# Kernel optimization log

Hardware: AMD Instinct MI355X
Metric: run time of the kernel (lower is better)

Reference implementation:

```python
import jax, jax.numpy as jnp
import numpy as np

NEG_INF = -9e15
ALPHA = 0.2  # LeakyReLU negative slope
OUT_FEATURES = 128


def setup_inputs() -> dict:
    key = jax.random.key(0)
    k1, k2, k3, k4 = jax.random.split(key, 4)
    B, N, F_in, F_out = 4, 4096, 256, OUT_FEATURES
    h = jax.random.normal(k1, (B, N, F_in), dtype=jnp.float32)
    adj = jax.random.randint(k2, (B, N, N), 0, 2, dtype=jnp.int32)
    W = jax.random.normal(k3, (F_in, F_out), dtype=jnp.float32) * 0.07
    a = jax.random.normal(k4, (2 * F_out, 1), dtype=jnp.float32) * 0.1
    return {"h": h, "adj": adj, "W": W, "a": a}


def reference(h, adj, W, a):
    # Wh: (B, N, F_out)
    Wh = jnp.einsum('bni,io->bno', h, W)
    a1 = a[:OUT_FEATURES, 0]   # (F_out,)
    a2 = a[OUT_FEATURES:, 0]   # (F_out,)
    Wh1 = Wh @ a1              # (B, N)
    Wh2 = Wh @ a2              # (B, N)
    e = Wh1[:, :, None] + Wh2[:, None, :]          # (B, N, N)
    e = jnp.where(e >= 0, e, ALPHA * e)             # LeakyReLU
    e = jnp.where(adj > 0, e, NEG_INF)              # adjacency mask
    attention = jax.nn.softmax(e, axis=-1)          # (B, N, N)
    # dropout omitted: reference runs in eval mode (training=False)
    h_prime = jnp.einsum('bnm,bmo->bno', attention, Wh)
    return jax.nn.elu(h_prime)  # concat=True
```

## Files before the change

### kernel.cpp

```cpp
#include <hip/hip_runtime.h>
#include <hip/hip_bf16.h>
#include <math.h>

typedef __attribute__((ext_vector_type(4))) float  f32x4;
typedef __attribute__((ext_vector_type(4))) int    i32x4;
typedef __attribute__((ext_vector_type(4))) unsigned u32x4;
typedef __attribute__((ext_vector_type(8))) short  s16x8;
typedef __attribute__((ext_vector_type(4))) short  s16x4;
typedef __attribute__((ext_vector_type(8))) __bf16 bf16x8;

#define LOG2E 1.4426950408889634f

__device__ __forceinline__ short f32_to_bf16_rne(float f) {
    unsigned u = __builtin_bit_cast(unsigned, f);
    u += 0x7fffu + ((u >> 16) & 1u);
    return (short)(u >> 16);
}
__device__ __forceinline__ int pack2_bf16(float f0, float f1) {
    unsigned u0 = __builtin_bit_cast(unsigned, f0) + 0x8000u;
    unsigned u1 = __builtin_bit_cast(unsigned, f1) + 0x8000u;
    return (int)((u0 >> 16) | (u1 & 0xffff0000u));
}
__device__ __forceinline__ bf16x8 as_bf16x8(s16x8 v) {
    return __builtin_bit_cast(bf16x8, v);
}
__device__ __forceinline__ bf16x8 as_bf16x8(i32x4 v) {
    return __builtin_bit_cast(bf16x8, v);
}

__global__ void k_pack(const int* __restrict__ adj, unsigned* __restrict__ bits) {
    long t = (long)blockIdx.x * 256 + threadIdx.x;
    const int* src = adj + t * 32;
    unsigned m = 0;
    #pragma unroll
    for (int c = 0; c < 8; ++c) {
        i32x4 v = *(const i32x4*)(src + c * 4);
        #pragma unroll
        for (int j = 0; j < 4; ++j)
            m |= (v[j] != 0) ? (1u << (c * 4 + j)) : 0u;
    }
    bits[t] = m;
}

__global__ void k0_wt(const float* __restrict__ W, short* __restrict__ WT) {
    int g = blockIdx.x * 256 + threadIdx.x;
    int col = g >> 6;
    int k0 = (g & 63) * 4;
    s16x4 v;
    #pragma unroll
    for (int i = 0; i < 4; ++i) v[i] = f32_to_bf16_rne(W[(k0 + i) * 128 + col]);
    *(s16x4*)(WT + col * 256 + k0) = v;
}

__global__ __launch_bounds__(256, 2) void k1_gemm(
    const float* __restrict__ h, const float* __restrict__ a,
    const short* __restrict__ WT,
    short* __restrict__ WhT, float* __restrict__ Wh1p, float* __restrict__ Tp)
{
    int l = threadIdx.x & 63;
    int w = threadIdx.x >> 6;
    int gw = blockIdx.x * 4 + w;
    int r0 = gw * 16;
    int lm = l & 15, q = l >> 4;

    f32x4 acc[8];
    #pragma unroll
    for (int ct = 0; ct < 8; ++ct) acc[ct] = (f32x4)0.0f;

    const float* hrow = h + (long)(r0 + lm) * 256;
    for (int kb = 0; kb < 8; ++kb) {
        int kbase = kb * 32 + q * 8;
        f32x4 h0 = *(const f32x4*)(hrow + kbase);
        f32x4 h1 = *(const f32x4*)(hrow + kbase + 4);
        s16x8 af;
        #pragma unroll
        for (int j = 0; j < 4; ++j) af[j] = f32_to_bf16_rne(h0[j]);
        #pragma unroll
        for (int j = 0; j < 4; ++j) af[4 + j] = f32_to_bf16_rne(h1[j]);
        bf16x8 afb = as_bf16x8(af);
        #pragma unroll
        for (int ct = 0; ct < 8; ++ct) {
            s16x8 bf = *(const s16x8*)(WT + (ct * 16 + lm) * 256 + kbase);
            acc[ct] = __builtin_amdgcn_mfma_f32_16x16x32_bf16(afb, as_bf16x8(bf), acc[ct], 0, 0, 0);
        }
    }

    int b = r0 >> 12;
    int nb = r0 & 4095;
    float p1[4] = {0.f, 0.f, 0.f, 0.f}, p2[4] = {0.f, 0.f, 0.f, 0.f};
    #pragma unroll
    for (int ct = 0; ct < 8; ++ct) {
        int col = ct * 16 + lm;
        float a1c = a[col], a2c = a[128 + col];
        s16x4 vv;
        #pragma unroll
        for (int r = 0; r < 4; ++r) {
            float v = acc[ct][r];
            p1[r] += v * a1c;
            p2[r] += v * a2c;
            vv[r] = f32_to_bf16_rne(v);
        }
        *(s16x4*)(WhT + ((long)(b * 128 + col) * 4096 + nb + q * 4)) = vv;
    }
    #pragma unroll
    for (int off = 1; off < 16; off <<= 1) {
        #pragma unroll
        for (int r = 0; r < 4; ++r) {
            p1[r] += __shfl_xor(p1[r], off);
            p2[r] += __shfl_xor(p2[r], off);
        }
    }
    if (lm == 0) {
        #pragma unroll
        for (int r = 0; r < 4; ++r) {
            int row = r0 + q * 4 + r;
            Wh1p[row] = LOG2E * p1[r];
            Tp[row]   = LOG2E * p2[r];
        }
    }
}

__global__ void k2_tmax(const float* __restrict__ Tp, float* __restrict__ Tmax) {
    __shared__ float red[256];
    int b = blockIdx.x, t = threadIdx.x;
    float mx = -1e30f;
    for (int i = 0; i < 16; ++i) mx = fmaxf(mx, Tp[b * 4096 + t + i * 256]);
    red[t] = mx;
    __syncthreads();
    for (int s = 128; s > 0; s >>= 1) {
        if (t < s) red[t] = fmaxf(red[t], red[t + s]);
        __syncthreads();
    }
    if (t == 0) Tmax[b] = red[0];
}

template <int SPLIT>
__global__ __launch_bounds__(256, 2) void k3_attn(
    const unsigned* __restrict__ bits, const short* __restrict__ WhT,
    const float* __restrict__ Wh1p, const float* __restrict__ Tp,
    const float* __restrict__ Tmax,
    float* __restrict__ U, float* __restrict__ Z)
{
    const int MSLICE = 4096 / SPLIT;
    const int MTILES = MSLICE / 128;
    __shared__ __align__(16) short tile[2][128 * 128];
    __shared__ __align__(16) float tps[4096 / SPLIT];

    int l = threadIdx.x & 63, w = threadIdx.x >> 6;
    int lm = l & 15, q = l >> 4;
    int bid = blockIdx.x;
    int mh = bid & (SPLIT - 1);
    int rg = (bid / SPLIT) & 63;
    int b  = bid / (SPLIT * 64);
    int n0 = rg * 64;
    int mbase = mh * MSLICE;

    int n_lane = n0 + w * 16 + lm;
    float sp = Wh1p[b * 4096 + n_lane];
    float xm = sp + Tmax[b];
    float Mrow = fmaxf(xm, 0.2f * xm);

    const unsigned* bitrow = bits + ((long)(b * 4096 + n_lane)) * 128 + mbase / 32;
    const short* whtb   = WhT + (long)b * 128 * 4096;
    const float* tpsq   = tps + q * 8;

    {
        const float* tg = Tp + b * 4096 + mbase;
        int i0 = threadIdx.x * 4;
        *(f32x4*)(tps + i0)        = *(const f32x4*)(tg + i0);
        *(f32x4*)(tps + i0 + 1024) = *(const f32x4*)(tg + i0 + 1024);
    }

    f32x4 acc[8];
    #pragma unroll
    for (int ct = 0; ct < 8; ++ct) acc[ct] = (f32x4)0.0f;
    float z = 0.0f;

    auto stage = [&](short* dst, int m0) {
        int colw = w * 32;
        #pragma unroll
        for (int j = 0; j < 8; ++j) {
            int cb = colw + j * 4;
            int col = cb + q;
            int gch = lm ^ (col & 7);
            const short* gp = whtb + (long)col * 4096 + m0 + gch * 8;
            __builtin_amdgcn_global_load_lds(
                (const __attribute__((address_space(1))) void*)gp,
                (__attribute__((address_space(3))) void*)(dst + cb * 128), 16, 0, 0);
        }
    };
    auto compute = [&](const short* buf, u32x4 bw, int mrel) {
        #pragma unroll
        for (int ks = 0; ks < 4; ++ks) {
            f32x4 t0 = *(const f32x4*)(tpsq + mrel + ks * 32);
            f32x4 t1 = *(const f32x4*)(tpsq + mrel + ks * 32 + 4);
            unsigned mq = bw[ks] >> (q * 8);
            i32x4 pk;
            float zs = 0.0f;
            #pragma unroll
            for (int half = 0; half < 2; ++half) {
                f32x4 t4 = half ? t1 : t0;
                float wv[4];
                #pragma unroll
                for (int j = 0; j < 4; ++j) {
                    float y = sp + t4[j];
                    float e = fmaxf(y, 0.2f * y) - Mrow;
                    float v = __builtin_amdgcn_exp2f(e);
                    v = (mq & (1u << (half * 4 + j))) ? v : 0.0f;
                    zs += v; wv[j] = v;
                }
                pk[half * 2]     = pack2_bf16(wv[0], wv[1]);
                pk[half * 2 + 1] = pack2_bf16(wv[2], wv[3]);
            }
            z += zs;
            bf16x8 ab = as_bf16x8(pk);
            #pragma unroll
            for (int ct = 0; ct < 8; ++ct) {
                int col = ct * 16 + lm;
                int pos = (ks * 4 + q) ^ (col & 7);
                s16x8 bf = *(const s16x8*)(buf + col * 128 + pos * 8);
                acc[ct] = __builtin_amdgcn_mfma_f32_16x16x32_bf16(ab, as_bf16x8(bf), acc[ct], 0, 0, 0);
            }
        }
    };

    u32x4 bwA, bwB;
    stage(tile[0], mbase);
    bwA = *(const u32x4*)(bitrow);
    __syncthreads();

    #pragma unroll 1
    for (int t = 0; t < MTILES; t += 2) {
        int r1 = (t + 1) & (MTILES - 1);
        stage(tile[1], mbase + r1 * 128);
        bwB = *(const u32x4*)(bitrow + r1 * 4);
        __builtin_amdgcn_sched_barrier(0);
        compute(tile[0], bwA, t * 128);
        __syncthreads();
        int r2 = (t + 2) & (MTILES - 1);
        stage(tile[0], mbase + r2 * 128);
        bwA = *(const u32x4*)(bitrow + r2 * 4);
        __builtin_amdgcn_sched_barrier(0);
        compute(tile[1], bwB, r1 * 128);
        __syncthreads();
    }

    z += __shfl_xor(z, 16);
    z += __shfl_xor(z, 32);

    int slice = b * SPLIT + mh;
    if (l < 16) Z[slice * 4096 + n0 + w * 16 + lm] = z;
    float* ub = U + ((long)slice * 4096 + n0 + w * 16) * 128;
    #pragma unroll
    for (int ct = 0; ct < 8; ++ct) {
        int col = ct * 16 + lm;
        #pragma unroll
        for (int r = 0; r < 4; ++r)
            ub[(q * 4 + r) * 128 + col] = acc[ct][r];
    }
}

__global__ void k4_combine(const float* __restrict__ U, const float* __restrict__ Z,
                           float* __restrict__ out) {
    long g = (long)blockIdx.x * 256 + threadIdx.x;
    long off = g * 4;
    long nf = off >> 7;
    int b = (int)(nf >> 12), n = (int)(nf & 4095), col = (int)(off & 127);
    long base0 = ((long)(b * 2) * 4096 + n) * 128 + col;
    f32x4 u0 = *(const f32x4*)(U + base0);
    f32x4 u1 = *(const f32x4*)(U + base0 + (long)4096 * 128);
    float zz = Z[(b * 2) * 4096 + n] + Z[(b * 2 + 1) * 4096 + n];
    f32x4 v;
    #pragma unroll
    for (int i = 0; i < 4; ++i) {
        float x = (u0[i] + u1[i]) / zz;
        v[i] = (x > 0.f) ? x : (expf(x) - 1.0f);
    }
    *(f32x4*)(out + off) = v;
}

extern "C" void kernel_launch(void* const* d_in, const int* in_sizes, int n_in,
                              void* d_out, int out_size, void* d_ws, size_t ws_size,
                              hipStream_t stream) {
    const float* h   = (const float*)d_in[0];
    const int*   adj = (const int*)d_in[1];
    const float* W   = (const float*)d_in[2];
    const float* a   = (const float*)d_in[3];
    float* out = (float*)d_out;

    char* ws = (char*)d_ws;
    short*    WhT  = (short*)ws;
    short*    WT   = (short*)(ws + 4194304);
    float*    Wh1p = (float*)(ws + 4259840);
    float*    Tp   = (float*)(ws + 4325376);
    float*    Tmax = (float*)(ws + 4390912);
    float*    U    = (float*)(ws + 4391168);
    float*    Z    = (float*)(ws + 4391168 + 16777216);
    unsigned* bits = (unsigned*)(ws + 4391168 + 16777216 + 131072);

    k_pack<<<8192, 256, 0, stream>>>(adj, bits);
    k0_wt<<<32, 256, 0, stream>>>(W, WT);
    k1_gemm<<<256, 256, 0, stream>>>(h, a, WT, WhT, Wh1p, Tp);
    k2_tmax<<<4, 256, 0, stream>>>(Tp, Tmax);
    k3_attn<2><<<512, 256, 0, stream>>>(bits, WhT, Wh1p, Tp, Tmax, U, Z);
    k4_combine<<<2048, 256, 0, stream>>>(U, Z, out);
    (void)in_sizes; (void)n_in; (void)out_size; (void)ws_size;
}
```

Baseline: 438.2 us.

## Switch attention kernel to 32x32 MFMA tiles with 8-way split and ballot packing

The attention kernel now uses 32x32x16 bf16 MFMA over 128-row blocks with 64-wide m tiles, splits the m dimension 8 ways instead of 2, and raises launch bounds to 4 blocks per CU. The adjacency bit-packing kernel now builds masks with wave ballots on coalesced per-lane loads instead of per-thread strided vector reads. The combine kernel sums 8 partial slices. The goal is better occupancy, more MFMA work per LDS fetch and cheaper mask packing, at the cost of a 4x larger partial-sum buffer and extra reduction traffic.

```diff
diff --git a/kernel.cpp b/kernel.cpp
--- a/kernel.cpp
+++ b/kernel.cpp
@@ -2,12 +2,14 @@
 #include <hip/hip_bf16.h>
 #include <math.h>
 
-typedef __attribute__((ext_vector_type(4))) float  f32x4;
-typedef __attribute__((ext_vector_type(4))) int    i32x4;
-typedef __attribute__((ext_vector_type(4))) unsigned u32x4;
-typedef __attribute__((ext_vector_type(8))) short  s16x8;
-typedef __attribute__((ext_vector_type(4))) short  s16x4;
-typedef __attribute__((ext_vector_type(8))) __bf16 bf16x8;
+typedef __attribute__((ext_vector_type(2))) float    f32x2;
+typedef __attribute__((ext_vector_type(4))) float    f32x4;
+typedef __attribute__((ext_vector_type(16))) float   f32x16;
+typedef __attribute__((ext_vector_type(4))) int      i32x4;
+typedef __attribute__((ext_vector_type(2))) unsigned u32x2;
+typedef __attribute__((ext_vector_type(8))) short    s16x8;
+typedef __attribute__((ext_vector_type(4))) short    s16x4;
+typedef __attribute__((ext_vector_type(8))) __bf16   bf16x8;
 
 #define LOG2E 1.4426950408889634f
 
@@ -29,17 +31,15 @@
 }
 
 __global__ void k_pack(const int* __restrict__ adj, unsigned* __restrict__ bits) {
-    long t = (long)blockIdx.x * 256 + threadIdx.x;
-    const int* src = adj + t * 32;
-    unsigned m = 0;
-    #pragma unroll
-    for (int c = 0; c < 8; ++c) {
-        i32x4 v = *(const i32x4*)(src + c * 4);
-        #pragma unroll
-        for (int j = 0; j < 4; ++j)
-            m |= (v[j] != 0) ? (1u << (c * 4 + j)) : 0u;
-    }
-    bits[t] = m;
+    long wave = ((long)blockIdx.x * 256 + threadIdx.x) >> 6;
+    int l = threadIdx.x & 63;
+    const int* src = adj + wave * 256;
+    unsigned long long m[4];
+    #pragma unroll
+    for (int k = 0; k < 4; ++k)
+        m[k] = __ballot(src[k * 64 + l] != 0);
+    if (l < 8)
+        bits[wave * 8 + l] = (unsigned)(m[l >> 1] >> ((l & 1) * 32));
 }
 
 __global__ void k0_wt(const float* __restrict__ W, short* __restrict__ WT) {
@@ -135,128 +135,130 @@
 }
 
 template <int SPLIT>
-__global__ __launch_bounds__(256, 2) void k3_attn(
+__global__ __launch_bounds__(256, 4) void k3_attn(
     const unsigned* __restrict__ bits, const short* __restrict__ WhT,
     const float* __restrict__ Wh1p, const float* __restrict__ Tp,
     const float* __restrict__ Tmax,
     float* __restrict__ U, float* __restrict__ Z)
 {
     const int MSLICE = 4096 / SPLIT;
-    const int MTILES = MSLICE / 128;
-    __shared__ __align__(16) short tile[2][128 * 128];
-    __shared__ __align__(16) float tps[4096 / SPLIT];
+    const int MT = 64;
+    const int NT = MSLICE / MT;
+    __shared__ __align__(16) short tile[2][128 * MT];
+    __shared__ __align__(16) float tps[MSLICE];
 
     int l = threadIdx.x & 63, w = threadIdx.x >> 6;
-    int lm = l & 15, q = l >> 4;
+    int i31 = l & 31, h = l >> 5;
     int bid = blockIdx.x;
     int mh = bid & (SPLIT - 1);
-    int rg = (bid / SPLIT) & 63;
-    int b  = bid / (SPLIT * 64);
-    int n0 = rg * 64;
+    int rg = (bid >> 3) & 31;
+    int b  = bid >> 8;
+    int n0 = rg * 128;
     int mbase = mh * MSLICE;
 
-    int n_lane = n0 + w * 16 + lm;
+    int n_lane = n0 + w * 32 + i31;
     float sp = Wh1p[b * 4096 + n_lane];
     float xm = sp + Tmax[b];
     float Mrow = fmaxf(xm, 0.2f * xm);
 
     const unsigned* bitrow = bits + ((long)(b * 4096 + n_lane)) * 128 + mbase / 32;
-    const short* whtb   = WhT + (long)b * 128 * 4096;
-    const float* tpsq   = tps + q * 8;
+    const short* whtb = WhT + (long)b * 128 * 4096 + mbase;
 
     {
         const float* tg = Tp + b * 4096 + mbase;
-        int i0 = threadIdx.x * 4;
-        *(f32x4*)(tps + i0)        = *(const f32x4*)(tg + i0);
-        *(f32x4*)(tps + i0 + 1024) = *(const f32x4*)(tg + i0 + 1024);
-    }
-
-    f32x4 acc[8];
-    #pragma unroll
-    for (int ct = 0; ct < 8; ++ct) acc[ct] = (f32x4)0.0f;
+        int i0 = threadIdx.x * 2;
+        *(f32x2*)(tps + i0) = *(const f32x2*)(tg + i0);
+    }
+
+    f32x16 acc[4];
+    #pragma unroll
+    for (int ct = 0; ct < 4; ++ct) acc[ct] = (f32x16)0.0f;
     float z = 0.0f;
 
     auto stage = [&](short* dst, int m0) {
-        int colw = w * 32;
-        #pragma unroll
-        for (int j = 0; j < 8; ++j) {
-            int cb = colw + j * 4;
-            int col = cb + q;
-            int gch = lm ^ (col & 7);
+        #pragma unroll
+        for (int j = 0; j < 4; ++j) {
+            int cb = w * 32 + j * 8;
+            int col = cb + (l >> 3);
+            int gch = (l & 7) ^ (col & 7);
             const short* gp = whtb + (long)col * 4096 + m0 + gch * 8;
             __builtin_amdgcn_global_load_lds(
                 (const __attribute__((address_space(1))) void*)gp,
-                (__attribute__((address_space(3))) void*)(dst + cb * 128), 16, 0, 0);
+                (__attribute__((address_space(3))) void*)(dst + cb * MT), 16, 0, 0);
         }
     };
-    auto compute = [&](const short* buf, u32x4 bw, int mrel) {
+
+    auto compute = [&](const short* buf, u32x2 bv, int mrel) {
         #pragma unroll
         for (int ks = 0; ks < 4; ++ks) {
-            f32x4 t0 = *(const f32x4*)(tpsq + mrel + ks * 32);
-            f32x4 t1 = *(const f32x4*)(tpsq + mrel + ks * 32 + 4);
-            unsigned mq = bw[ks] >> (q * 8);
-            i32x4 pk;
+            int mt = ks * 16 + h * 8;
+            const float* tp8 = tps + mrel + mt;
+            f32x4 ta = *(const f32x4*)(tp8);
+            f32x4 tb = *(const f32x4*)(tp8 + 4);
+            unsigned wsel = (ks >= 2) ? bv[1] : bv[0];
+            unsigned mq = wsel >> ((ks & 1) * 16 + h * 8);
+            float wv[8];
             float zs = 0.0f;
             #pragma unroll
-            for (int half = 0; half < 2; ++half) {
-                f32x4 t4 = half ? t1 : t0;
-                float wv[4];
-                #pragma unroll
-                for (int j = 0; j < 4; ++j) {
-                    float y = sp + t4[j];
-                    float e = fmaxf(y, 0.2f * y) - Mrow;
-                    float v = __builtin_amdgcn_exp2f(e);
-                    v = (mq & (1u << (half * 4 + j))) ? v : 0.0f;
-                    zs += v; wv[j] = v;
-                }
-                pk[half * 2]     = pack2_bf16(wv[0], wv[1]);
-                pk[half * 2 + 1] = pack2_bf16(wv[2], wv[3]);
+            for (int j = 0; j < 8; ++j) {
+                float tt = (j < 4) ? ta[j] : tb[j - 4];
+                float y = sp + tt;
+                float e = fmaxf(y, 0.2f * y) - Mrow;
+                float v = __builtin_amdgcn_exp2f(e);
+                v = (mq & (1u << j)) ? v : 0.0f;
+                zs += v; wv[j] = v;
             }
             z += zs;
+            i32x4 pk;
+            pk[0] = pack2_bf16(wv[0], wv[1]);
+            pk[1] = pack2_bf16(wv[2], wv[3]);
+            pk[2] = pack2_bf16(wv[4], wv[5]);
+            pk[3] = pack2_bf16(wv[6], wv[7]);
             bf16x8 ab = as_bf16x8(pk);
             #pragma unroll
-            for (int ct = 0; ct < 8; ++ct) {
-                int col = ct * 16 + lm;
-                int pos = (ks * 4 + q) ^ (col & 7);
-                s16x8 bf = *(const s16x8*)(buf + col * 128 + pos * 8);
-                acc[ct] = __builtin_amdgcn_mfma_f32_16x16x32_bf16(ab, as_bf16x8(bf), acc[ct], 0, 0, 0);
+            for (int ct = 0; ct < 4; ++ct) {
+                int col = ct * 32 + i31;
+                int pos = (ks * 2 + h) ^ (col & 7);
+                s16x8 bf = *(const s16x8*)(buf + col * MT + pos * 8);
+                acc[ct] = __builtin_amdgcn_mfma_f32_32x32x16_bf16(ab, as_bf16x8(bf), acc[ct], 0, 0, 0);
             }
         }
     };
 
-    u32x4 bwA, bwB;
-    stage(tile[0], mbase);
-    bwA = *(const u32x4*)(bitrow);
+    u32x2 bvA, bvB;
+    stage(tile[0], 0);
+    bvA = *(const u32x2*)(bitrow);
     __syncthreads();
 
     #pragma unroll 1
-    for (int t = 0; t < MTILES; t += 2) {
-        int r1 = (t + 1) & (MTILES - 1);
-        stage(tile[1], mbase + r1 * 128);
-        bwB = *(const u32x4*)(bitrow + r1 * 4);
+    for (int t = 0; t < NT; t += 2) {
+        int r1 = (t + 1) & (NT - 1);
+        stage(tile[1], r1 * MT);
+        bvB = *(const u32x2*)(bitrow + r1 * 2);
         __builtin_amdgcn_sched_barrier(0);
-        compute(tile[0], bwA, t * 128);
+        compute(tile[0], bvA, t * MT);
         __syncthreads();
-        int r2 = (t + 2) & (MTILES - 1);
-        stage(tile[0], mbase + r2 * 128);
-        bwA = *(const u32x4*)(bitrow + r2 * 4);
+        int r2 = (t + 2) & (NT - 1);
+        stage(tile[0], r2 * MT);
+        bvA = *(const u32x2*)(bitrow + r2 * 2);
         __builtin_amdgcn_sched_barrier(0);
-        compute(tile[1], bwB, r1 * 128);
+        compute(tile[1], bvB, r1 * MT);
         __syncthreads();
     }
 
-    z += __shfl_xor(z, 16);
     z += __shfl_xor(z, 32);
 
     int slice = b * SPLIT + mh;
-    if (l < 16) Z[slice * 4096 + n0 + w * 16 + lm] = z;
-    float* ub = U + ((long)slice * 4096 + n0 + w * 16) * 128;
-    #pragma unroll
-    for (int ct = 0; ct < 8; ++ct) {
-        int col = ct * 16 + lm;
-        #pragma unroll
-        for (int r = 0; r < 4; ++r)
-            ub[(q * 4 + r) * 128 + col] = acc[ct][r];
+    if (l < 32) Z[slice * 4096 + n0 + w * 32 + l] = z;
+    float* ub = U + ((long)slice * 4096 + n0 + w * 32) * 128;
+    #pragma unroll
+    for (int ct = 0; ct < 4; ++ct) {
+        int col = ct * 32 + i31;
+        #pragma unroll
+        for (int r = 0; r < 16; ++r) {
+            int rowoff = (r & 3) + 8 * (r >> 2) + 4 * h;
+            ub[rowoff * 128 + col] = acc[ct][r];
+        }
     }
 }
 
@@ -266,14 +268,19 @@
     long off = g * 4;
     long nf = off >> 7;
     int b = (int)(nf >> 12), n = (int)(nf & 4095), col = (int)(off & 127);
-    long base0 = ((long)(b * 2) * 4096 + n) * 128 + col;
-    f32x4 u0 = *(const f32x4*)(U + base0);
-    f32x4 u1 = *(const f32x4*)(U + base0 + (long)4096 * 128);
-    float zz = Z[(b * 2) * 4096 + n] + Z[(b * 2 + 1) * 4096 + n];
+    const long slice = (long)4096 * 128;
+    long base0 = ((long)(b * 8) * 4096 + n) * 128 + col;
+    f32x4 s = (f32x4)0.0f;
+    float zz = 0.0f;
+    #pragma unroll
+    for (int i = 0; i < 8; ++i) {
+        s += *(const f32x4*)(U + base0 + i * slice);
+        zz += Z[(b * 8 + i) * 4096 + n];
+    }
     f32x4 v;
     #pragma unroll
     for (int i = 0; i < 4; ++i) {
-        float x = (u0[i] + u1[i]) / zz;
+        float x = s[i] / zz;
         v[i] = (x > 0.f) ? x : (expf(x) - 1.0f);
     }
     *(f32x4*)(out + off) = v;
@@ -295,14 +302,14 @@
     float*    Tp   = (float*)(ws + 4325376);
     float*    Tmax = (float*)(ws + 4390912);
     float*    U    = (float*)(ws + 4391168);
-    float*    Z    = (float*)(ws + 4391168 + 16777216);
-    unsigned* bits = (unsigned*)(ws + 4391168 + 16777216 + 131072);
-
-    k_pack<<<8192, 256, 0, stream>>>(adj, bits);
+    float*    Z    = (float*)(ws + 4391168 + 67108864);
+    unsigned* bits = (unsigned*)(ws + 4391168 + 67108864 + 524288);
+
+    k_pack<<<65536, 256, 0, stream>>>(adj, bits);
     k0_wt<<<32, 256, 0, stream>>>(W, WT);
     k1_gemm<<<256, 256, 0, stream>>>(h, a, WT, WhT, Wh1p, Tp);
     k2_tmax<<<4, 256, 0, stream>>>(Tp, Tmax);
-    k3_attn<2><<<512, 256, 0, stream>>>(bits, WhT, Wh1p, Tp, Tmax, U, Z);
+    k3_attn<8><<<1024, 256, 0, stream>>>(bits, WhT, Wh1p, Tp, Tmax, U, Z);
     k4_combine<<<2048, 256, 0, stream>>>(U, Z, out);
     (void)in_sizes; (void)n_in; (void)out_size; (void)ws_size;
 }
```

Measured after the change: 443.8 us. Within noise of the previous version (+1.3%).
